# Optimization experiments

Measured on AMD Instinct MI355X. Metric: run time of the kernel, lower is better.

Reference implementation:

```python
import jax, jax.numpy as jnp
import numpy as np

S_IN = 32      # input spatial size
KSZ = 3        # kernel size
STRIDE = 1
S_OUT = (S_IN - KSZ) // STRIDE + 1   # 30
C_IN = 16      # input capsule types
C_OUT = 32     # output capsule types
ROUTINGS = 3
EPS = 1e-7     # K.epsilon()


def _child_parent_map(size_in, size_out, kernel_size):
    # For each parent position, the flat indices of its kernel_size^2 children.
    cpm = np.zeros((size_out ** 2, kernel_size ** 2), dtype=np.int32)
    for p in range(size_out ** 2):
        idx = []
        for kr in range(kernel_size):
            start = kr * size_in + p % size_out + (p // size_out) * size_in
            idx.extend(range(start, start + kernel_size))
        cpm[p] = idx
    return cpm

_CPM = jnp.asarray(_child_parent_map(S_IN, S_OUT, KSZ))  # [S_OUT^2, KSZ^2]


def setup_inputs() -> dict:
    key = jax.random.key(0)
    k1, k2, k3, k4, k5 = jax.random.split(key, 5)
    return {
        "input_act": jax.random.uniform(k1, (S_IN, S_IN, C_IN, 1), dtype=jnp.float32),
        "input_pose": jax.random.normal(k2, (S_IN, S_IN, C_IN, 4, 4), dtype=jnp.float32),
        "transformation_weights": jax.random.normal(k3, (1, KSZ * KSZ * C_IN, C_OUT, 4, 4), dtype=jnp.float32) * 0.1,
        "beta_a": jax.random.normal(k4, (1, 1, C_OUT), dtype=jnp.float32),
        "beta_v": jax.random.normal(k5, (1, 1, C_OUT, 1), dtype=jnp.float32),
    }


def reference(input_act, input_pose, transformation_weights, beta_a, beta_v):
    P = S_OUT ** 2                 # parent positions
    N = KSZ * KSZ * C_IN           # children per parent

    pose = input_pose.reshape(S_IN ** 2, C_IN, 4, 4)
    act = input_act.reshape(S_IN ** 2, C_IN, 1)

    # gather children per parent position (irregular gather via child_parent_map)
    pose_f = pose[_CPM].reshape(P, N, 4, 4)        # [P, N, 4, 4]
    act_f = act[_CPM].reshape(P, N, 1, 1)          # [P, N, 1, 1] (broadcasts over C_OUT)

    W = transformation_weights[0]                  # [N, C_OUT, 4, 4]
    # votes[p,n,c,i,j] = sum_k pose_f[p,n,i,k] * W[n,c,k,j] (avoids K.tile materialization)
    votes = jnp.einsum('pnik,nckj->pncij', pose_f, W).reshape(P, N, C_OUT, 16)

    rr = jnp.full((P, N, C_OUT, 1), 1.0 / C_OUT, dtype=votes.dtype)

    out_act = None
    means = None
    for i in range(ROUTINGS):
        lambd = 0.01 * (1.0 - 0.95 ** i)
        # ---- M step ----
        rs = jnp.sum(rr, axis=1, keepdims=True)                              # [P,1,C,1]
        means = jnp.sum(rr * votes, axis=1, keepdims=True) / rs              # [P,1,C,16]
        var = jnp.sum(rr * jnp.square(votes - means), axis=1, keepdims=True) / rs
        std = jnp.sqrt(var)                                                  # [P,1,C,16]
        costs = beta_v + jnp.log(std + EPS) * rs                             # [P,1,C,16]
        out_act = jax.nn.sigmoid(lambd * (beta_a - jnp.sum(costs, axis=-1)))[..., None]  # [P,1,C,1]
        if i < ROUTINGS - 1:
            # ---- E step ----
            prob_exp = -jnp.sum(jnp.square(votes - means) / (2.0 * jnp.square(std)),
                                axis=-1, keepdims=True)                      # [P,N,C,1]
            prob_main = -jnp.sum(jnp.log(std + EPS), axis=-1, keepdims=True)  # [P,1,C,1]
            zz = jnp.log(out_act + EPS) + prob_main + prob_exp
            rr = jax.nn.softmax(zz, axis=0)                                   # softmax over parent axis, as in source

    out_act = out_act.reshape(S_OUT, S_OUT, C_OUT, 1)
    out_pose = means.reshape(S_OUT, S_OUT, C_OUT, 4, 4)
    return (out_act, out_pose)
```

## Files before the change

### kernel.cpp

```cpp
#include <hip/hip_runtime.h>


#define S_IN   32
#define S_OUT  30
#define PP     (S_OUT * S_OUT)
#define NN     144
#define NREP   16
#define PLSZ   (NN * 32)
#define EPSF   1e-7f
#define CLAMPA 80.0f

#define LOADW(dst, n_) do {                                              \
    const float4* _wp = (const float4*)&W[((n_) * 32 + c) * 16];         \
    float4 _w0 = _wp[0], _w1 = _wp[1], _w2 = _wp[2], _w3 = _wp[3];       \
    dst[0] = _w0.x; dst[1] = _w0.y; dst[2] = _w0.z; dst[3] = _w0.w;      \
    dst[4] = _w1.x; dst[5] = _w1.y; dst[6] = _w1.z; dst[7] = _w1.w;      \
    dst[8] = _w2.x; dst[9] = _w2.y; dst[10] = _w2.z; dst[11] = _w2.w;    \
    dst[12] = _w3.x; dst[13] = _w3.y; dst[14] = _w3.z; dst[15] = _w3.w;  \
} while (0)

#define LOADPO(dst, n_) do {                                             \
    const float4* _pp = (const float4*)&pose_s[(n_) * 16];               \
    float4 _p0 = _pp[0], _p1 = _pp[1], _p2 = _pp[2], _p3 = _pp[3];       \
    dst[0] = _p0.x; dst[1] = _p0.y; dst[2] = _p0.z; dst[3] = _p0.w;      \
    dst[4] = _p1.x; dst[5] = _p1.y; dst[6] = _p1.z; dst[7] = _p1.w;      \
    dst[8] = _p2.x; dst[9] = _p2.y; dst[10] = _p2.z; dst[11] = _p2.w;    \
    dst[12] = _p3.x; dst[13] = _p3.y; dst[14] = _p3.z; dst[15] = _p3.w;  \
} while (0)

#define VOTES(v_, po_, w_) do {                                          \
    _Pragma("unroll")                                                    \
    for (int _i = 0; _i < 4; ++_i) {                                     \
        float _p0 = po_[_i*4+0], _p1 = po_[_i*4+1];                      \
        float _p2 = po_[_i*4+2], _p3 = po_[_i*4+3];                      \
        _Pragma("unroll")                                                \
        for (int _j = 0; _j < 4; ++_j)                                   \
            v_[_i*4+_j] = fmaf(_p0, w_[_j], fmaf(_p1, w_[4+_j],          \
                          fmaf(_p2, w_[8+_j], _p3 * w_[12+_j])));        \
    }                                                                    \
} while (0)

__device__ __forceinline__ float sumrep(const float* __restrict__ cs, int idx) {
    float s0 = 0.f, s1 = 0.f, s2 = 0.f, s3 = 0.f;
#pragma unroll
    for (int r = 0; r < NREP; r += 4) {
        s0 += cs[(r + 0) * PLSZ + idx];
        s1 += cs[(r + 1) * PLSZ + idx];
        s2 += cs[(r + 2) * PLSZ + idx];
        s3 += cs[(r + 3) * PLSZ + idx];
    }
    return (s0 + s1) + (s2 + s3);
}

template <bool FIRST, bool LAST>
__global__ __launch_bounds__(256, 4) void me_kernel(
    const float* __restrict__ pose,
    const float* __restrict__ W,
    const float* __restrict__ beta_a,
    const float* __restrict__ beta_v,
    const float* __restrict__ csR,
    float* __restrict__ csW,
    float* __restrict__ meanw,
    float* __restrict__ i2vw,
    float* __restrict__ basew,
    float* __restrict__ out,
    float lambd)
{
    const int p = blockIdx.x;
    const int t = threadIdx.x;
    const int c = t & 31;
    const int slot = t >> 5;
    const int wave = t >> 6;
    const int rep = p & (NREP - 1);

    __shared__ float pose_s[NN * 16];
    __shared__ float red[33 * 4 * 32];
    __shared__ float mean_s[16 * 32];
    __shared__ float i2v_s[16 * 32];
    __shared__ float base_s[32];
    __shared__ float lg[4 * 32];

    const int prow = p / S_OUT, pcol = p % S_OUT;
    {
        const float4* pose4 = (const float4*)pose;
        float4* ps4 = (float4*)pose_s;
        for (int idx = t; idx < 576; idx += 256) {
            int kk = idx >> 6;
            int child = (prow + kk / 3) * S_IN + (pcol + kk % 3);
            ps4[idx] = pose4[child * 64 + (idx & 63)];
        }
    }

    float mn[16], iv[16], base = 0.f;
    if (!FIRST) {
        const float4* m4 = (const float4*)&meanw[(p * 32 + c) * 16];
        const float4* v4 = (const float4*)&i2vw[(p * 32 + c) * 16];
#pragma unroll
        for (int q = 0; q < 4; ++q) {
            float4 a = m4[q], b = v4[q];
            mn[q * 4 + 0] = a.x; mn[q * 4 + 1] = a.y; mn[q * 4 + 2] = a.z; mn[q * 4 + 3] = a.w;
            iv[q * 4 + 0] = b.x; iv[q * 4 + 1] = b.y; iv[q * 4 + 2] = b.z; iv[q * 4 + 3] = b.w;
        }
        base = basew[p * 32 + c];
    }
    __syncthreads();

    float rsum = 0.f;
    float s1[16], s2[16];
#pragma unroll
    for (int q = 0; q < 16; ++q) { s1[q] = 0.f; s2[q] = 0.f; }

    float w[16];
    LOADW(w, slot);
    float cs = 1.f;
    if (!FIRST) cs = sumrep(csR, slot * 32 + c);

    for (int k = 0; k < 18; ++k) {
        const int n = (k << 3) + slot;
        float po[16];
        LOADPO(po, n);
        float v[16];
        VOTES(v, po, w);
        float cs_next = cs;
        if (k < 17) {
            LOADW(w, n + 8);
            if (!FIRST) cs_next = sumrep(csR, (n + 8) * 32 + c);
        }
        if (FIRST) {
#pragma unroll
            for (int q = 0; q < 16; ++q) {
                s1[q] += v[q];
                s2[q] = fmaf(v[q], v[q], s2[q]);
            }
        } else {
            float pe = 0.f;
#pragma unroll
            for (int q = 0; q < 16; ++q) {
                float d = v[q] - mn[q];
                pe = fmaf(d * d, iv[q], pe);
            }
            float r = __expf(fminf(base - pe, CLAMPA)) * __builtin_amdgcn_rcpf(cs);
#pragma unroll
            for (int q = 0; q < 16; ++q) {
                s1[q] = fmaf(r, v[q], s1[q]);
                float rv = r * v[q];
                s2[q] = fmaf(rv, v[q], s2[q]);
            }
            rsum += r;
        }
        cs = cs_next;
    }

#pragma unroll
    for (int q = 0; q < 16; ++q) {
        s1[q] += __shfl_xor(s1[q], 32);
        s2[q] += __shfl_xor(s2[q], 32);
    }
    rsum += __shfl_xor(rsum, 32);

    if ((t & 32) == 0) {
#pragma unroll
        for (int q = 0; q < 16; ++q) {
            red[(q * 4 + wave) * 32 + c] = s1[q];
            red[((16 + q) * 4 + wave) * 32 + c] = s2[q];
        }
        red[(32 * 4 + wave) * 32 + c] = rsum;
    }
    __syncthreads();

    if (t < 128) {
        const int qq = t >> 5, cl = t & 31;
        float rs, inv_rs;
        if (FIRST) {
            rs = 4.5f;
            inv_rs = 1.0f / 144.0f;
        } else {
            rs = red[(32 * 4 + 0) * 32 + cl] + red[(32 * 4 + 1) * 32 + cl] +
                 red[(32 * 4 + 2) * 32 + cl] + red[(32 * 4 + 3) * 32 + cl];
            inv_rs = 1.0f / rs;
        }
        float lsum = 0.f;
        float mq[4], vq[4];
#pragma unroll
        for (int u = 0; u < 4; ++u) {
            const int q = qq * 4 + u;
            float a1 = red[(q * 4 + 0) * 32 + cl] + red[(q * 4 + 1) * 32 + cl] +
                       red[(q * 4 + 2) * 32 + cl] + red[(q * 4 + 3) * 32 + cl];
            float a2 = red[((16 + q) * 4 + 0) * 32 + cl] + red[((16 + q) * 4 + 1) * 32 + cl] +
                       red[((16 + q) * 4 + 2) * 32 + cl] + red[((16 + q) * 4 + 3) * 32 + cl];
            float m = a1 * inv_rs;
            float var = fmaxf(a2 * inv_rs - m * m, 1e-30f);
            float sd = __builtin_sqrtf(var);
            mq[u] = m;
            vq[u] = 0.5f / var;
            lsum += __logf(sd + EPSF);
            mean_s[q * 32 + cl] = m;
            i2v_s[q * 32 + cl] = vq[u];
        }
        lg[qq * 32 + cl] = lsum;
        float4 mv; mv.x = mq[0]; mv.y = mq[1]; mv.z = mq[2]; mv.w = mq[3];
        if (LAST) {
            ((float4*)(out + PP * 32))[(p * 32 + cl) * 4 + qq] = mv;
        } else {
            float4 vv; vv.x = vq[0]; vv.y = vq[1]; vv.z = vq[2]; vv.w = vq[3];
            ((float4*)meanw)[(p * 32 + cl) * 4 + qq] = mv;
            ((float4*)i2vw)[(p * 32 + cl) * 4 + qq] = vv;
        }
    }
    __syncthreads();

    if (t < 32) {
        float rs = FIRST ? 4.5f
                 : red[(32 * 4 + 0) * 32 + c] + red[(32 * 4 + 1) * 32 + c] +
                   red[(32 * 4 + 2) * 32 + c] + red[(32 * 4 + 3) * 32 + c];
        float lsum = lg[c] + lg[32 + c] + lg[64 + c] + lg[96 + c];
        float sumcosts = 16.f * beta_v[c] + rs * lsum;
        float a = 1.0f / (1.0f + __expf(-(lambd * (beta_a[c] - sumcosts))));
        if (LAST) {
            out[p * 32 + c] = a;
        } else {
            float b = __logf(a + EPSF) - lsum;
            basew[p * 32 + c] = b;
            base_s[c] = b;
        }
    }

    if (!LAST) {
        __syncthreads();
        float tbase = base_s[c];
#pragma unroll
        for (int q = 0; q < 16; ++q) {
            mn[q] = mean_s[q * 32 + c];
            iv[q] = i2v_s[q * 32 + c];
        }
        LOADW(w, slot);
        float* csp = csW + rep * PLSZ;
        for (int k = 0; k < 18; ++k) {
            const int n = (k << 3) + slot;
            float po[16];
            LOADPO(po, n);
            float v[16];
            VOTES(v, po, w);
            if (k < 17) LOADW(w, n + 8);
            float pe = 0.f;
#pragma unroll
            for (int q = 0; q < 16; ++q) {
                float d = v[q] - mn[q];
                pe = fmaf(d * d, iv[q], pe);
            }
            float e = __expf(fminf(tbase - pe, CLAMPA));
            atomicAdd(&csp[n * 32 + c], e);
        }
    }
}

extern "C" void kernel_launch(void* const* d_in, const int* in_sizes, int n_in,
                              void* d_out, int out_size, void* d_ws, size_t ws_size,
                              hipStream_t stream) {
    const float* pose   = (const float*)d_in[1];
    const float* W      = (const float*)d_in[2];
    const float* beta_a = (const float*)d_in[3];
    const float* beta_v = (const float*)d_in[4];
    float* out = (float*)d_out;
    float* ws = (float*)d_ws;

    float* meanw = ws;
    float* i2vw  = meanw + PP * 32 * 16;
    float* basew = i2vw + PP * 32 * 16;
    float* cs0   = basew + PP * 32;
    float* cs1   = cs0 + NREP * PLSZ;

    const float lambd0 = 0.0f;
    const float lambd1 = 0.01f * (1.0f - 0.95f);
    const float lambd2 = 0.01f * (1.0f - 0.95f * 0.95f);

    hipMemsetAsync(cs0, 0, 2 * NREP * PLSZ * sizeof(float), stream);

    me_kernel<true, false><<<PP, 256, 0, stream>>>(
        pose, W, beta_a, beta_v, cs0, cs0, meanw, i2vw, basew, out, lambd0);
    me_kernel<false, false><<<PP, 256, 0, stream>>>(
        pose, W, beta_a, beta_v, cs0, cs1, meanw, i2vw, basew, out, lambd1);
    me_kernel<false, true><<<PP, 256, 0, stream>>>(
        pose, W, beta_a, beta_v, cs1, nullptr, meanw, i2vw, basew, out, lambd2);
}
```

Measured before the change: 145.1 us.

## Collapse replica planes in a separate kernel and double threads per block

Each parent block previously re-summed the 16 replica planes of the softmax denominator for every child it touched. A small collapse kernel now reduces the planes once into a single array between M/E passes, so the main kernel reads one value per entry. The main kernel also runs 512 threads per block, with 16 slots over the 144 children instead of 8, which halves the per-thread loop length and widens the shared-memory reduction. The cost is two extra kernel launches, and the larger blocks may lower occupancy per compute unit.

```diff
diff --git a/kernel.cpp b/kernel.cpp
--- a/kernel.cpp
+++ b/kernel.cpp
@@ -40,25 +40,13 @@
     }                                                                    \
 } while (0)
 
-__device__ __forceinline__ float sumrep(const float* __restrict__ cs, int idx) {
-    float s0 = 0.f, s1 = 0.f, s2 = 0.f, s3 = 0.f;
-#pragma unroll
-    for (int r = 0; r < NREP; r += 4) {
-        s0 += cs[(r + 0) * PLSZ + idx];
-        s1 += cs[(r + 1) * PLSZ + idx];
-        s2 += cs[(r + 2) * PLSZ + idx];
-        s3 += cs[(r + 3) * PLSZ + idx];
-    }
-    return (s0 + s1) + (s2 + s3);
-}
-
 template <bool FIRST, bool LAST>
-__global__ __launch_bounds__(256, 4) void me_kernel(
+__global__ __launch_bounds__(512, 4) void me_kernel(
     const float* __restrict__ pose,
     const float* __restrict__ W,
     const float* __restrict__ beta_a,
     const float* __restrict__ beta_v,
-    const float* __restrict__ csR,
+    const float* __restrict__ csC,
     float* __restrict__ csW,
     float* __restrict__ meanw,
     float* __restrict__ i2vw,
@@ -74,7 +62,7 @@
     const int rep = p & (NREP - 1);
 
     __shared__ float pose_s[NN * 16];
-    __shared__ float red[33 * 4 * 32];
+    __shared__ float red[33 * 8 * 32];
     __shared__ float mean_s[16 * 32];
     __shared__ float i2v_s[16 * 32];
     __shared__ float base_s[32];
@@ -84,7 +72,7 @@
     {
         const float4* pose4 = (const float4*)pose;
         float4* ps4 = (float4*)pose_s;
-        for (int idx = t; idx < 576; idx += 256) {
+        for (int idx = t; idx < 576; idx += 512) {
             int kk = idx >> 6;
             int child = (prow + kk / 3) * S_IN + (pcol + kk % 3);
             ps4[idx] = pose4[child * 64 + (idx & 63)];
@@ -113,18 +101,18 @@
     float w[16];
     LOADW(w, slot);
     float cs = 1.f;
-    if (!FIRST) cs = sumrep(csR, slot * 32 + c);
-
-    for (int k = 0; k < 18; ++k) {
-        const int n = (k << 3) + slot;
+    if (!FIRST) cs = csC[slot * 32 + c];
+
+    for (int k = 0; k < 9; ++k) {
+        const int n = (k << 4) + slot;
         float po[16];
         LOADPO(po, n);
         float v[16];
         VOTES(v, po, w);
         float cs_next = cs;
-        if (k < 17) {
-            LOADW(w, n + 8);
-            if (!FIRST) cs_next = sumrep(csR, (n + 8) * 32 + c);
+        if (k < 8) {
+            LOADW(w, n + 16);
+            if (!FIRST) cs_next = csC[(n + 16) * 32 + c];
         }
         if (FIRST) {
 #pragma unroll
@@ -161,10 +149,10 @@
     if ((t & 32) == 0) {
 #pragma unroll
         for (int q = 0; q < 16; ++q) {
-            red[(q * 4 + wave) * 32 + c] = s1[q];
-            red[((16 + q) * 4 + wave) * 32 + c] = s2[q];
-        }
-        red[(32 * 4 + wave) * 32 + c] = rsum;
+            red[(q * 8 + wave) * 32 + c] = s1[q];
+            red[((16 + q) * 8 + wave) * 32 + c] = s2[q];
+        }
+        red[(32 * 8 + wave) * 32 + c] = rsum;
     }
     __syncthreads();
 
@@ -175,8 +163,9 @@
             rs = 4.5f;
             inv_rs = 1.0f / 144.0f;
         } else {
-            rs = red[(32 * 4 + 0) * 32 + cl] + red[(32 * 4 + 1) * 32 + cl] +
-                 red[(32 * 4 + 2) * 32 + cl] + red[(32 * 4 + 3) * 32 + cl];
+            rs = 0.f;
+#pragma unroll
+            for (int w8 = 0; w8 < 8; ++w8) rs += red[(32 * 8 + w8) * 32 + cl];
             inv_rs = 1.0f / rs;
         }
         float lsum = 0.f;
@@ -184,10 +173,12 @@
 #pragma unroll
         for (int u = 0; u < 4; ++u) {
             const int q = qq * 4 + u;
-            float a1 = red[(q * 4 + 0) * 32 + cl] + red[(q * 4 + 1) * 32 + cl] +
-                       red[(q * 4 + 2) * 32 + cl] + red[(q * 4 + 3) * 32 + cl];
-            float a2 = red[((16 + q) * 4 + 0) * 32 + cl] + red[((16 + q) * 4 + 1) * 32 + cl] +
-                       red[((16 + q) * 4 + 2) * 32 + cl] + red[((16 + q) * 4 + 3) * 32 + cl];
+            float a1 = 0.f, a2 = 0.f;
+#pragma unroll
+            for (int w8 = 0; w8 < 8; ++w8) {
+                a1 += red[(q * 8 + w8) * 32 + cl];
+                a2 += red[((16 + q) * 8 + w8) * 32 + cl];
+            }
             float m = a1 * inv_rs;
             float var = fmaxf(a2 * inv_rs - m * m, 1e-30f);
             float sd = __builtin_sqrtf(var);
@@ -210,9 +201,14 @@
     __syncthreads();
 
     if (t < 32) {
-        float rs = FIRST ? 4.5f
-                 : red[(32 * 4 + 0) * 32 + c] + red[(32 * 4 + 1) * 32 + c] +
-                   red[(32 * 4 + 2) * 32 + c] + red[(32 * 4 + 3) * 32 + c];
+        float rs;
+        if (FIRST) {
+            rs = 4.5f;
+        } else {
+            rs = 0.f;
+#pragma unroll
+            for (int w8 = 0; w8 < 8; ++w8) rs += red[(32 * 8 + w8) * 32 + c];
+        }
         float lsum = lg[c] + lg[32 + c] + lg[64 + c] + lg[96 + c];
         float sumcosts = 16.f * beta_v[c] + rs * lsum;
         float a = 1.0f / (1.0f + __expf(-(lambd * (beta_a[c] - sumcosts))));
@@ -235,13 +231,13 @@
         }
         LOADW(w, slot);
         float* csp = csW + rep * PLSZ;
-        for (int k = 0; k < 18; ++k) {
-            const int n = (k << 3) + slot;
+        for (int k = 0; k < 9; ++k) {
+            const int n = (k << 4) + slot;
             float po[16];
             LOADPO(po, n);
             float v[16];
             VOTES(v, po, w);
-            if (k < 17) LOADW(w, n + 8);
+            if (k < 8) LOADW(w, n + 16);
             float pe = 0.f;
 #pragma unroll
             for (int q = 0; q < 16; ++q) {
@@ -252,6 +248,22 @@
             atomicAdd(&csp[n * 32 + c], e);
         }
     }
+}
+
+__global__ __launch_bounds__(256) void collapse_kernel(
+    const float* __restrict__ planes, float* __restrict__ csum)
+{
+    const int idx = blockIdx.x * 256 + threadIdx.x;
+    if (idx >= PLSZ) return;
+    float s0 = 0.f, s1 = 0.f, s2 = 0.f, s3 = 0.f;
+#pragma unroll
+    for (int r = 0; r < NREP; r += 4) {
+        s0 += planes[(r + 0) * PLSZ + idx];
+        s1 += planes[(r + 1) * PLSZ + idx];
+        s2 += planes[(r + 2) * PLSZ + idx];
+        s3 += planes[(r + 3) * PLSZ + idx];
+    }
+    csum[idx] = (s0 + s1) + (s2 + s3);
 }
 
 extern "C" void kernel_launch(void* const* d_in, const int* in_sizes, int n_in,
@@ -264,22 +276,28 @@
     float* out = (float*)d_out;
     float* ws = (float*)d_ws;
 
-    float* meanw = ws;
-    float* i2vw  = meanw + PP * 32 * 16;
-    float* basew = i2vw + PP * 32 * 16;
-    float* cs0   = basew + PP * 32;
-    float* cs1   = cs0 + NREP * PLSZ;
+    float* meanw   = ws;
+    float* i2vw    = meanw + PP * 32 * 16;
+    float* basew   = i2vw + PP * 32 * 16;
+    float* planes0 = basew + PP * 32;
+    float* planes1 = planes0 + NREP * PLSZ;
+    float* csum0   = planes1 + NREP * PLSZ;
+    float* csum1   = csum0 + PLSZ;
 
     const float lambd0 = 0.0f;
     const float lambd1 = 0.01f * (1.0f - 0.95f);
     const float lambd2 = 0.01f * (1.0f - 0.95f * 0.95f);
 
-    hipMemsetAsync(cs0, 0, 2 * NREP * PLSZ * sizeof(float), stream);
-
-    me_kernel<true, false><<<PP, 256, 0, stream>>>(
-        pose, W, beta_a, beta_v, cs0, cs0, meanw, i2vw, basew, out, lambd0);
-    me_kernel<false, false><<<PP, 256, 0, stream>>>(
-        pose, W, beta_a, beta_v, cs0, cs1, meanw, i2vw, basew, out, lambd1);
-    me_kernel<false, true><<<PP, 256, 0, stream>>>(
-        pose, W, beta_a, beta_v, cs1, nullptr, meanw, i2vw, basew, out, lambd2);
+    const int cg = (PLSZ + 255) / 256;
+
+    hipMemsetAsync(planes0, 0, 2 * NREP * PLSZ * sizeof(float), stream);
+
+    me_kernel<true, false><<<PP, 512, 0, stream>>>(
+        pose, W, beta_a, beta_v, csum0, planes0, meanw, i2vw, basew, out, lambd0);
+    collapse_kernel<<<cg, 256, 0, stream>>>(planes0, csum0);
+    me_kernel<false, false><<<PP, 512, 0, stream>>>(
+        pose, W, beta_a, beta_v, csum0, planes1, meanw, i2vw, basew, out, lambd1);
+    collapse_kernel<<<cg, 256, 0, stream>>>(planes1, csum1);
+    me_kernel<false, true><<<PP, 512, 0, stream>>>(
+        pose, W, beta_a, beta_v, csum1, nullptr, meanw, i2vw, basew, out, lambd2);
 }
```

After: 122.7 us. 15.5% less time.
